# Kernel optimization log

Measured on AMD Instinct MI355X. Metric: run time of the kernel, lower is better.

The kernel has to match this reference:

```python
import jax, jax.numpy as jnp
import numpy as np


def _bilinear_ac(img, H, W):
    """Bilinear resize with align_corners=True. img: [B, C, h, w] -> [B, C, H, W]."""
    B, C, h, w = img.shape
    ys = jnp.linspace(0.0, h - 1.0, H)
    xs = jnp.linspace(0.0, w - 1.0, W)
    y0 = jnp.floor(ys).astype(jnp.int32)
    x0 = jnp.floor(xs).astype(jnp.int32)
    y1 = jnp.minimum(y0 + 1, h - 1)
    x1 = jnp.minimum(x0 + 1, w - 1)
    wy = (ys - y0).astype(img.dtype)  # [H]
    wx = (xs - x0).astype(img.dtype)  # [W]
    top = img[:, :, y0, :]            # [B, C, H, w]
    bot = img[:, :, y1, :]
    row = top * (1.0 - wy)[None, None, :, None] + bot * wy[None, None, :, None]
    left = row[:, :, :, x0]           # [B, C, H, W]
    right = row[:, :, :, x1]
    return left * (1.0 - wx)[None, None, None, :] + right * wx[None, None, None, :]


def setup_inputs() -> dict:
    key = jax.random.key(0)
    k1, k2, k3 = jax.random.split(key, 3)
    B, F, h, w = 16, 256, 64, 64
    H, W = 512, 512
    K = 21
    feature_map = jax.random.normal(k1, (B, F, h, w), dtype=jnp.float32)
    x = jax.random.uniform(k2, (B, 3, H, W), dtype=jnp.float32)
    conv_w = jax.random.normal(k3, (K, F), dtype=jnp.float32) * 0.05
    conv_b = jnp.zeros((K,), dtype=jnp.float32)
    return {"feature_map": feature_map, "x": x, "conv_w": conv_w, "conv_b": conv_b}


def reference(feature_map, x, conv_w, conv_b):
    B, _, H, W = x.shape
    # 1x1 conv: feature_dim -> num_classes
    logits = jnp.einsum('bfhw,kf->bkhw', feature_map, conv_w) + conv_b[None, :, None, None]
    seg = jax.nn.softmax(logits, axis=1)                 # [B, K, h, w]
    seg = _bilinear_ac(seg, H, W)                        # [B, K, H, W]
    xp = jnp.transpose(x, (0, 2, 3, 1))                  # [B, H, W, C]
    # per-class masked mean pooling (the python loop, fused into one einsum)
    q = jnp.einsum('bhwc,bkhw->bkc', xp, seg) / (H * W)  # [B, K, C]
    # broadcast dot-product attention maps
    attn = jnp.einsum('bhwc,bkc->bkhw', xp, q)           # [B, K, H, W]
    return attn
```

## Files before the change

### kernel.cpp

```cpp
#include <hip/hip_runtime.h>

#define BN 16
#define FD 256
#define SH 64
#define SW 64
#define BH 512
#define BW 512
#define KN 21
#define SP (SH*SW)
#define BP (BH*BW)

#define SEG_BLOCKS 256
#define DOWNX_BLOCKS (BN*3*BH/4)

typedef float f32x4 __attribute__((ext_vector_type(4)));

__device__ __forceinline__ float adj_w(int big, int small) {
    float t = (float)big * (63.0f / 511.0f);
    int i0 = (int)t;
    float fr = t - (float)i0;
    int i1 = i0 + 1; if (i1 > 63) i1 = 63;
    float w = 0.0f;
    if (i0 == small) w += 1.0f - fr;
    if (i1 == small) w += fr;
    return w;
}

__device__ __forceinline__ void adj_range(int small, int& lo, int& hi) {
    lo = (int)floorf((small - 1) * (511.0f / 63.0f)); if (lo < 0) lo = 0;
    hi = (int)ceilf((small + 1) * (511.0f / 63.0f));  if (hi > 511) hi = 511;
}

__device__ __forceinline__ void seg_body(int blk, int tid,
                                         const float* __restrict__ fm,
                                         const float* __restrict__ cw,
                                         const float* __restrict__ cb,
                                         float* __restrict__ seg) {
    int gid = blk * 256 + tid;
    int b   = gid >> 12;
    int p   = gid & 4095;
    const float* fmb = fm + (size_t)b * FD * SP + p;

    float acc[KN];
#pragma unroll
    for (int k = 0; k < KN; ++k) acc[k] = 0.0f;

#pragma unroll 4
    for (int f = 0; f < FD; ++f) {
        float v = fmb[(size_t)f * SP];
#pragma unroll
        for (int k = 0; k < KN; ++k)
            acc[k] = fmaf(v, cw[k * FD + f], acc[k]);
    }

    float mx = -1e30f;
#pragma unroll
    for (int k = 0; k < KN; ++k) { acc[k] += cb[k]; mx = fmaxf(mx, acc[k]); }
    float s = 0.0f;
#pragma unroll
    for (int k = 0; k < KN; ++k) { acc[k] = expf(acc[k] - mx); s += acc[k]; }
    float inv = 1.0f / s;

    float* segb = seg + (size_t)b * KN * SP + p;
#pragma unroll
    for (int k = 0; k < KN; ++k) segb[(size_t)k * SP] = acc[k] * inv;
}

__device__ __forceinline__ void downx_body(int blk, int tid,
                                           const float* __restrict__ x,
                                           float* __restrict__ tmpA,
                                           float (*rows)[BW]) {
    int bc = blk >> 7;
    int Y0 = (blk & 127) << 2;
    const f32x4* src = (const f32x4*)(x + ((size_t)bc * BH + Y0) * BW);
    f32x4* dst = (f32x4*)&rows[0][0];
    dst[tid]       = src[tid];
    dst[tid + 256] = src[tid + 256];
    __syncthreads();

    int s  = tid & 63;
    int yl = tid >> 6;
    int lo, hi; adj_range(s, lo, hi);
    float acc = 0.0f;
    for (int X = lo; X <= hi; ++X) acc = fmaf(adj_w(X, s), rows[yl][X], acc);
    tmpA[((size_t)bc * BH + Y0 + yl) * SW + s] = acc;
}

__global__ __launch_bounds__(256) void k_phase1(const float* __restrict__ fm,
                                                const float* __restrict__ cw,
                                                const float* __restrict__ cb,
                                                const float* __restrict__ x,
                                                float* __restrict__ seg,
                                                float* __restrict__ tmpA) {
    __shared__ float rows[4][BW];
    if (blockIdx.x < SEG_BLOCKS) seg_body(blockIdx.x, threadIdx.x, fm, cw, cb, seg);
    else                         downx_body(blockIdx.x - SEG_BLOCKS, threadIdx.x, x, tmpA, rows);
}

__global__ __launch_bounds__(256) void k_downyq(const float* __restrict__ tmpA,
                                                const float* __restrict__ seg,
                                                float* __restrict__ q) {
    int bc = blockIdx.x;
    int b  = bc / 3, c = bc - b * 3;
    const float* base = tmpA + (size_t)bc * BH * SW;
    const float* segb = seg + (size_t)b * KN * SP;

    float qk[KN];
#pragma unroll
    for (int k = 0; k < KN; ++k) qk[k] = 0.0f;

    for (int i = 0; i < SP / 256; ++i) {
        int p = i * 256 + threadIdx.x;
        int r = p >> 6, s = p & 63;
        int lo, hi; adj_range(r, lo, hi);
        float xv = 0.0f;
        for (int Y = lo; Y <= hi; ++Y)
            xv = fmaf(adj_w(Y, r), base[(size_t)Y * SW + s], xv);
#pragma unroll
        for (int k = 0; k < KN; ++k)
            qk[k] = fmaf(segb[(size_t)k * SP + p], xv, qk[k]);
    }

    __shared__ float red[4][KN];
    int lane = threadIdx.x & 63, w = threadIdx.x >> 6;
#pragma unroll
    for (int k = 0; k < KN; ++k) {
        float v = qk[k];
        for (int off = 32; off > 0; off >>= 1) v += __shfl_down(v, off, 64);
        if (lane == 0) red[w][k] = v;
    }
    __syncthreads();
    if (threadIdx.x < KN) {
        float v = red[0][threadIdx.x] + red[1][threadIdx.x]
                + red[2][threadIdx.x] + red[3][threadIdx.x];
        q[((size_t)b * KN + threadIdx.x) * 3 + c] = v * (1.0f / (float)BP);
    }
}

__global__ __launch_bounds__(256) void k_attn(const float* __restrict__ x,
                                              const float* __restrict__ q,
                                              float* __restrict__ out) {
    int b   = blockIdx.x >> 8;
    int blk = blockIdx.x & 255;
    int p4  = blk * 256 + threadIdx.x;

    const f32x4* xb = (const f32x4*)(x + (size_t)b * 3 * BP);
    f32x4 x0 = xb[p4];
    f32x4 x1 = xb[BP / 4 + p4];
    f32x4 x2 = xb[2 * (BP / 4) + p4];

    __shared__ float qs[KN * 3];
    if (threadIdx.x < KN * 3) qs[threadIdx.x] = q[(size_t)b * KN * 3 + threadIdx.x];
    __syncthreads();

    f32x4* ob = (f32x4*)(out + (size_t)b * KN * BP) + p4;
#pragma unroll
    for (int k = 0; k < KN; ++k) {
        float q0 = qs[k * 3], q1 = qs[k * 3 + 1], q2 = qs[k * 3 + 2];
        f32x4 r = x0 * q0 + x1 * q1 + x2 * q2;
        ob[(size_t)k * (BP / 4)] = r;
    }
}

extern "C" void kernel_launch(void* const* d_in, const int* in_sizes, int n_in,
                              void* d_out, int out_size, void* d_ws, size_t ws_size,
                              hipStream_t stream) {
    const float* fm = (const float*)d_in[0];
    const float* x  = (const float*)d_in[1];
    const float* cw = (const float*)d_in[2];
    const float* cb = (const float*)d_in[3];
    float* out = (float*)d_out;

    float* seg  = (float*)d_ws;
    float* tmpA = seg  + (size_t)BN * KN * SP;
    float* q    = tmpA + (size_t)BN * 3 * BH * SW;

    k_phase1<<<SEG_BLOCKS + DOWNX_BLOCKS, 256, 0, stream>>>(fm, cw, cb, x, seg, tmpA);
    k_downyq<<<BN * 3,                    256, 0, stream>>>(tmpA, seg, q);
    k_attn  <<<BN * (BP / 1024),          256, 0, stream>>>(x, q, out);
}
```

Measured before the change: 565.0 us.

## Split q reduction across spatial parts with atomics, use nontemporal output stores

The per-(batch,channel) q reduction kernel, which launched only 48 blocks, is restructured into 256 blocks that each handle one batch and a 256-pixel slice for all three channels. Each block downsamples x for its slice into shared memory, reduces over seg, and atomically adds partial sums into q, which phase1 now zeroes. This is meant to remove the low-occupancy serial loop in the reduction stage and to read seg once per pixel instead of three times. Separately, the attention output stores become nontemporal to reduce cache pollution on the large write. Atomics make the float summation order nondeterministic.

```diff
diff --git a/kernel.cpp b/kernel.cpp
--- a/kernel.cpp
+++ b/kernel.cpp
@@ -12,6 +12,7 @@
 
 #define SEG_BLOCKS 256
 #define DOWNX_BLOCKS (BN*3*BH/4)
+#define QPARTS 16
 
 typedef float f32x4 __attribute__((ext_vector_type(4)));
 
@@ -91,49 +92,64 @@
                                                 const float* __restrict__ cb,
                                                 const float* __restrict__ x,
                                                 float* __restrict__ seg,
-                                                float* __restrict__ tmpA) {
+                                                float* __restrict__ tmpA,
+                                                float* __restrict__ q) {
     __shared__ float rows[4][BW];
+    if (blockIdx.x < 4) {
+        int i = blockIdx.x * 256 + threadIdx.x;
+        if (i < BN * KN * 3) q[i] = 0.0f;
+    }
     if (blockIdx.x < SEG_BLOCKS) seg_body(blockIdx.x, threadIdx.x, fm, cw, cb, seg);
     else                         downx_body(blockIdx.x - SEG_BLOCKS, threadIdx.x, x, tmpA, rows);
 }
 
-__global__ __launch_bounds__(256) void k_downyq(const float* __restrict__ tmpA,
+__global__ __launch_bounds__(256) void k_phase2(const float* __restrict__ tmpA,
                                                 const float* __restrict__ seg,
                                                 float* __restrict__ q) {
-    int bc = blockIdx.x;
-    int b  = bc / 3, c = bc - b * 3;
-    const float* base = tmpA + (size_t)bc * BH * SW;
-    const float* segb = seg + (size_t)b * KN * SP;
+    int b    = blockIdx.x >> 4;
+    int part = blockIdx.x & 15;
+    int p0   = part * 256;
 
-    float qk[KN];
+    __shared__ float xd[3][256];
+    for (int e = threadIdx.x; e < 3 * 256; e += 256) {
+        int c = e >> 8;
+        int j = e & 255;
+        int p = p0 + j;
+        int r = p >> 6, s = p & 63;
+        const float* base = tmpA + ((size_t)(b * 3 + c) * BH) * SW + s;
+        int lo, hi; adj_range(r, lo, hi);
+        float acc = 0.0f;
+        for (int Y = lo; Y <= hi; ++Y) acc = fmaf(adj_w(Y, r), base[(size_t)Y * SW], acc);
+        xd[c][j] = acc;
+    }
+    __syncthreads();
+
+    const float* segb = seg + (size_t)b * KN * SP + p0 + threadIdx.x;
+    float x0 = xd[0][threadIdx.x], x1 = xd[1][threadIdx.x], x2 = xd[2][threadIdx.x];
+    float accq[KN][3];
 #pragma unroll
-    for (int k = 0; k < KN; ++k) qk[k] = 0.0f;
-
-    for (int i = 0; i < SP / 256; ++i) {
-        int p = i * 256 + threadIdx.x;
-        int r = p >> 6, s = p & 63;
-        int lo, hi; adj_range(r, lo, hi);
-        float xv = 0.0f;
-        for (int Y = lo; Y <= hi; ++Y)
-            xv = fmaf(adj_w(Y, r), base[(size_t)Y * SW + s], xv);
-#pragma unroll
-        for (int k = 0; k < KN; ++k)
-            qk[k] = fmaf(segb[(size_t)k * SP + p], xv, qk[k]);
+    for (int k = 0; k < KN; ++k) {
+        float sv = segb[(size_t)k * SP];
+        accq[k][0] = sv * x0;
+        accq[k][1] = sv * x1;
+        accq[k][2] = sv * x2;
     }
 
-    __shared__ float red[4][KN];
+    __shared__ float redq[4][KN * 3];
     int lane = threadIdx.x & 63, w = threadIdx.x >> 6;
 #pragma unroll
-    for (int k = 0; k < KN; ++k) {
-        float v = qk[k];
-        for (int off = 32; off > 0; off >>= 1) v += __shfl_down(v, off, 64);
-        if (lane == 0) red[w][k] = v;
-    }
+    for (int k = 0; k < KN; ++k)
+#pragma unroll
+        for (int c = 0; c < 3; ++c) {
+            float v = accq[k][c];
+            for (int off = 32; off > 0; off >>= 1) v += __shfl_down(v, off, 64);
+            if (lane == 0) redq[w][k * 3 + c] = v;
+        }
     __syncthreads();
-    if (threadIdx.x < KN) {
-        float v = red[0][threadIdx.x] + red[1][threadIdx.x]
-                + red[2][threadIdx.x] + red[3][threadIdx.x];
-        q[((size_t)b * KN + threadIdx.x) * 3 + c] = v * (1.0f / (float)BP);
+    if (threadIdx.x < KN * 3) {
+        float v = redq[0][threadIdx.x] + redq[1][threadIdx.x]
+                + redq[2][threadIdx.x] + redq[3][threadIdx.x];
+        atomicAdd(q + (size_t)b * KN * 3 + threadIdx.x, v * (1.0f / (float)BP));
     }
 }
 
@@ -158,7 +174,7 @@
     for (int k = 0; k < KN; ++k) {
         float q0 = qs[k * 3], q1 = qs[k * 3 + 1], q2 = qs[k * 3 + 2];
         f32x4 r = x0 * q0 + x1 * q1 + x2 * q2;
-        ob[(size_t)k * (BP / 4)] = r;
+        __builtin_nontemporal_store(r, ob + (size_t)k * (BP / 4));
     }
 }
 
@@ -175,7 +191,7 @@
     float* tmpA = seg  + (size_t)BN * KN * SP;
     float* q    = tmpA + (size_t)BN * 3 * BH * SW;
 
-    k_phase1<<<SEG_BLOCKS + DOWNX_BLOCKS, 256, 0, stream>>>(fm, cw, cb, x, seg, tmpA);
-    k_downyq<<<BN * 3,                    256, 0, stream>>>(tmpA, seg, q);
+    k_phase1<<<SEG_BLOCKS + DOWNX_BLOCKS, 256, 0, stream>>>(fm, cw, cb, x, seg, tmpA, q);
+    k_phase2<<<BN * QPARTS,               256, 0, stream>>>(tmpA, seg, q);
     k_attn  <<<BN * (BP / 1024),          256, 0, stream>>>(x, q, out);
 }
```

Measured after the change: 493.6 us. 12.6% less time.
